# Performance work log

Measured on AMD Instinct MI355X. Metric: run time of the kernel, lower is better.

Reference implementation:

```python
import jax, jax.numpy as jnp
import numpy as np

B, T, D, H, V, L = 2, 1024, 512, 8, 50257, 4
HD = D // H  # head size
FF = 4 * D


def _ln(x, w, b):
    mu = jnp.mean(x, axis=-1, keepdims=True)
    var = jnp.mean((x - mu) ** 2, axis=-1, keepdims=True)
    return (x - mu) * jax.lax.rsqrt(var + 1e-5) * w + b


def setup_inputs() -> dict:
    key = jax.random.key(0)
    ks = jax.random.split(key, 12)
    s = 0.02
    return {
        "idx": jax.random.randint(ks[0], (B, T), 0, V),
        "tok_emb": jax.random.normal(ks[1], (V, D)) * s,
        "pos_emb": jax.random.normal(ks[2], (T, D)) * s,
        "Wq": jax.random.normal(ks[3], (L, H, D, HD)) * s,
        "Wk": jax.random.normal(ks[4], (L, H, D, HD)) * s,
        "Wv": jax.random.normal(ks[5], (L, H, D, HD)) * s,
        "Wo": jax.random.normal(ks[6], (L, D, D)) * s,
        "bo": jnp.zeros((L, D)),
        "W1": jax.random.normal(ks[7], (L, D, FF)) * s,
        "b1": jnp.zeros((L, FF)),
        "W2": jax.random.normal(ks[8], (L, FF, D)) * s,
        "b2": jnp.zeros((L, D)),
        "ln1_w": jnp.ones((L, D)), "ln1_b": jnp.zeros((L, D)),
        "ln2_w": jnp.ones((L, D)), "ln2_b": jnp.zeros((L, D)),
        "Wlm": jax.random.normal(ks[9], (D, V)) * s,
        "blm": jnp.zeros((V,)),
    }


def reference(idx, tok_emb, pos_emb, Wq, Wk, Wv, Wo, bo, W1, b1, W2, b2,
              ln1_w, ln1_b, ln2_w, ln2_b, Wlm, blm):
    b, t = idx.shape
    x = tok_emb[idx] + pos_emb[:t]  # [B,T,D]
    mask = jnp.tril(jnp.ones((t, t), dtype=bool))
    scale = D ** (-0.5)  # NOTE: original scales by full n_embd, not head_size
    for l in range(L):
        # pre-norm that also feeds the residual (x = ln1(x); x = x + sa(x))
        h = _ln(x, ln1_w[l], ln1_b[l])
        q = jnp.einsum('btd,hdk->bhtk', h, Wq[l])
        k = jnp.einsum('btd,hdk->bhtk', h, Wk[l])
        v = jnp.einsum('btd,hdk->bhtk', h, Wv[l])
        wei = jnp.einsum('bhtk,bhsk->bhts', q, k) * scale
        wei = jnp.where(mask, wei, -jnp.inf)
        wei = jax.nn.softmax(wei, axis=-1)  # dropout omitted (eval mode)
        att = jnp.einsum('bhts,bhsk->bhtk', wei, v)
        att = att.transpose(0, 2, 1, 3).reshape(b, t, D)  # concat heads
        x = h + att @ Wo[l] + bo[l]
        h2 = _ln(x, ln2_w[l], ln2_b[l])
        x = h2 + jax.nn.relu(h2 @ W1[l] + b1[l]) @ W2[l] + b2[l]
    logits = x @ Wlm + blm  # [B,T,V]
    return logits
```

## Files before the change

kernel.cpp:

```cpp
#include <hip/hip_runtime.h>
#include <hip/hip_bf16.h>

typedef __hip_bfloat16 bf16;
typedef __attribute__((ext_vector_type(8))) short s8v;
typedef __attribute__((ext_vector_type(4))) float f4v;

#define B_ 2
#define T_ 1024
#define D_ 512
#define H_ 8
#define HD_ 64
#define V_ 50257
#define VPAD_ 51200
#define L_ 4
#define FF_ 2048
#define BT_ (B_*T_)

__device__ __forceinline__ float ldw(const void* p, size_t i, int f32m) {
  return f32m ? ((const float*)p)[i] : __bfloat162float(((const bf16*)p)[i]);
}

__device__ __forceinline__ void gload_lds16(const void* g, void* l) {
  __builtin_amdgcn_global_load_lds((const __attribute__((address_space(1))) void*)g,
                                   (__attribute__((address_space(3))) void*)l, 16, 0, 0);
}

__global__ void detect_kernel(const void* __restrict__ ln1w, int* __restrict__ flag) {
  unsigned u = *(const unsigned*)ln1w;
  *flag = (u == 0x3F800000u) ? 1 : 0;
}

__global__ void embed_kernel(const int* __restrict__ idx, const void* __restrict__ tok,
                             const void* __restrict__ pos, float* __restrict__ x,
                             const int* __restrict__ flag) {
  int f32m = *flag;
  int i = blockIdx.x * 256 + threadIdx.x;
  int bt = i >> 9;
  int d  = i & (D_ - 1);
  int t  = bt & (T_ - 1);
  int tk = idx[bt];
  x[i] = ldw(tok, (size_t)tk * D_ + d, f32m) + ldw(pos, (size_t)t * D_ + d, f32m);
}

__global__ void ln_kernel(const float* __restrict__ x, const void* __restrict__ w,
                          const void* __restrict__ b, size_t eoff,
                          bf16* __restrict__ hb, float* __restrict__ hf,
                          const int* __restrict__ flag) {
  int f32m = *flag;
  int t = blockIdx.x;
  int tid = threadIdx.x;
  const float* row = x + (size_t)t * D_;
  float v0 = row[tid], v1 = row[tid + 256];
  __shared__ float red[256];
  red[tid] = v0 + v1;
  __syncthreads();
  for (int s = 128; s > 0; s >>= 1) { if (tid < s) red[tid] += red[tid + s]; __syncthreads(); }
  float mu = red[0] * (1.f / D_);
  __syncthreads();
  float d0 = v0 - mu, d1 = v1 - mu;
  red[tid] = d0 * d0 + d1 * d1;
  __syncthreads();
  for (int s = 128; s > 0; s >>= 1) { if (tid < s) red[tid] += red[tid + s]; __syncthreads(); }
  float rs = rsqrtf(red[0] * (1.f / D_) + 1e-5f);
  float o0 = d0 * rs * ldw(w, eoff + tid, f32m)       + ldw(b, eoff + tid, f32m);
  float o1 = d1 * rs * ldw(w, eoff + tid + 256, f32m) + ldw(b, eoff + tid + 256, f32m);
  size_t base = (size_t)t * D_;
  hf[base + tid] = o0;        hf[base + tid + 256] = o1;
  hb[base + tid] = __float2bfloat16(o0);
  hb[base + tid + 256] = __float2bfloat16(o1);
}

__global__ void repack_qkv_all_kernel(const void* __restrict__ Wq, const void* __restrict__ Wk,
                                      const void* __restrict__ Wv, bf16* __restrict__ out,
                                      const int* __restrict__ flag) {
  int f32m = *flag;
  int zz = blockIdx.z;
  size_t eoff = (size_t)zz * H_ * D_ * HD_;
  out += (size_t)zz * 1536 * 512;
  int i = blockIdx.x * 256 + threadIdx.x;
  int n = i >> 9, k = i & 511;
  int sel = n >> 9; int cc = n & 511; int hh = cc >> 6; int hd = cc & 63;
  const void* src = (sel == 0) ? Wq : (sel == 1) ? Wk : Wv;
  out[i] = __float2bfloat16(ldw(src, eoff + ((size_t)hh * D_ + k) * HD_ + hd, f32m));
}

__global__ void repack_qkv_kernel(const void* __restrict__ Wq, const void* __restrict__ Wk,
                                  const void* __restrict__ Wv, size_t eoff,
                                  bf16* __restrict__ out, const int* __restrict__ flag) {
  int f32m = *flag;
  int i = blockIdx.x * 256 + threadIdx.x;
  int n = i >> 9, k = i & 511;
  int sel = n >> 9; int cc = n & 511; int hh = cc >> 6; int hd = cc & 63;
  const void* src = (sel == 0) ? Wq : (sel == 1) ? Wk : Wv;
  out[i] = __float2bfloat16(ldw(src, eoff + ((size_t)hh * D_ + k) * HD_ + hd, f32m));
}

__global__ void transpose_kernel(const void* __restrict__ in, size_t eoff,
                                 bf16* __restrict__ out, int K, int Nin,
                                 const int* __restrict__ flag) {
  int f32m = *flag;
  __shared__ bf16 tl[32][33];
  int n0 = blockIdx.x * 32, k0 = blockIdx.y * 32;
  int tx = threadIdx.x & 31, ty = threadIdx.x >> 5;
#pragma unroll
  for (int i = 0; i < 4; ++i) {
    int k = k0 + ty + i * 8;
    int n = n0 + tx;
    float v = (n < Nin) ? ldw(in, eoff + (size_t)k * Nin + n, f32m) : 0.f;
    tl[ty + i * 8][tx] = __float2bfloat16(v);
  }
  __syncthreads();
#pragma unroll
  for (int i = 0; i < 4; ++i) {
    int n = n0 + ty + i * 8;
    out[(size_t)n * K + k0 + tx] = tl[tx][ty + i * 8];
  }
}

__global__ void transpose_all_kernel(const void* __restrict__ in,
                                     bf16* __restrict__ out,
                                     int K, int Nin, const int* __restrict__ flag) {
  int f32m = *flag;
  int zz = blockIdx.z;
  size_t eoff = (size_t)zz * K * Nin;
  out += (size_t)zz * Nin * K;
  __shared__ bf16 tl[32][33];
  int n0 = blockIdx.x * 32, k0 = blockIdx.y * 32;
  int tx = threadIdx.x & 31, ty = threadIdx.x >> 5;
#pragma unroll
  for (int i = 0; i < 4; ++i) {
    int k = k0 + ty + i * 8;
    int n = n0 + tx;
    tl[ty + i * 8][tx] = __float2bfloat16(ldw(in, eoff + (size_t)k * Nin + n, f32m));
  }
  __syncthreads();
#pragma unroll
  for (int i = 0; i < 4; ++i) {
    int n = n0 + ty + i * 8;
    out[(size_t)n * K + k0 + tx] = tl[tx][ty + i * 8];
  }
}

template<int OUTM, int BIAS, int RES, int RELU, int XB>
__global__ __launch_bounds__(256)
void mfma_gemm64(const bf16* __restrict__ A, const bf16* __restrict__ Bt,
                 void* __restrict__ Cout, const void* __restrict__ bias, size_t bieoff,
                 const float* __restrict__ res, bf16* __restrict__ xb2,
                 const int* __restrict__ flag, int M, int Nc, int K) {
  __shared__ __align__(16) short As[2][2048];
  __shared__ __align__(16) short Bs[2][2048];
  const int tid = threadIdx.x;
  const int brow = blockIdx.x * 64;
  const int bcol = blockIdx.y * 64;
  const int w = tid >> 6, lane = tid & 63;
  const int wr = w >> 1, wc = w & 1;
  const int lr = lane & 15, lk = lane >> 4;

  const int e0 = tid * 8;
  const int r0 = e0 >> 5;
  const int c0 = (e0 & 31) ^ ((r0 & 3) << 3);
  const bf16* ag0 = A + (size_t)(brow + r0) * K + c0;
  const bf16* bg0 = Bt + (size_t)(bcol + r0) * K + c0;

  int aoff[2], boff[2];
#pragma unroll
  for (int i = 0; i < 2; ++i) {
    int ra = wr * 32 + i * 16 + lr;
    aoff[i] = ra * 32 + ((lk * 8) ^ ((lr & 3) << 3));
    int rb = wc * 32 + i * 16 + lr;
    boff[i] = rb * 32 + ((lk * 8) ^ ((lr & 3) << 3));
  }

  f4v acc[2][2];
  const f4v z = {0.f, 0.f, 0.f, 0.f};
#pragma unroll
  for (int i = 0; i < 2; ++i)
#pragma unroll
    for (int j = 0; j < 2; ++j) acc[i][j] = z;

  const int nt = K >> 5;
  gload_lds16(ag0, &As[0][e0]);
  gload_lds16(bg0, &Bs[0][e0]);

  for (int kt = 0; kt < nt; ++kt) {
    __syncthreads();
    const int cur = kt & 1;
    if (kt + 1 < nt) {
      const size_t ko = (size_t)(kt + 1) * 32;
      gload_lds16(ag0 + ko, &As[cur ^ 1][e0]);
      gload_lds16(bg0 + ko, &Bs[cur ^ 1][e0]);
    }
    s8v a[2], b[2];
#pragma unroll
    for (int i = 0; i < 2; ++i) a[i] = *(const s8v*)&As[cur][aoff[i]];
#pragma unroll
    for (int i = 0; i < 2; ++i) b[i] = *(const s8v*)&Bs[cur][boff[i]];
#pragma unroll
    for (int mi = 0; mi < 2; ++mi)
#pragma unroll
      for (int ni = 0; ni < 2; ++ni)
        acc[mi][ni] = __builtin_amdgcn_mfma_f32_16x16x32_bf16(a[mi], b[ni], acc[mi][ni], 0, 0, 0);
  }

  const int f32m = *flag;
#pragma unroll
  for (int mi = 0; mi < 2; ++mi) {
    const int row = brow + wr * 32 + mi * 16 + lk * 4;
#pragma unroll
    for (int ni = 0; ni < 2; ++ni) {
      const int col = bcol + wc * 32 + ni * 16 + lr;
      if (col < Nc) {
        float bv = BIAS ? ldw(bias, bieoff + col, f32m) : 0.f;
#pragma unroll
        for (int rr = 0; rr < 4; ++rr) {
          float v = acc[mi][ni][rr] + bv;
          size_t ci = (size_t)(row + rr) * Nc + col;
          if (RES) v += res[ci];
          if (RELU) v = fmaxf(v, 0.f);
          if (OUTM == 0) ((float*)Cout)[ci] = v;
          else           ((bf16*)Cout)[ci] = __float2bfloat16(v);
          if (XB) xb2[ci] = __float2bfloat16(v);
        }
      }
    }
  }
}

__global__ __launch_bounds__(256)
void mfma_gemm_lm(const bf16* __restrict__ A, const bf16* __restrict__ Bt,
                  void* __restrict__ Cout, const void* __restrict__ bias,
                  const int* __restrict__ flag, int M, int Nc, int K) {
  __shared__ __align__(16) short As[2][4096];
  __shared__ __align__(16) short Bs[2][4096];
  const int bid = blockIdx.x;
  const int g = bid >> 3;
  const int brow = (g & 15) * 128;
  const int bcol = ((bid & 7) * 50 + (g >> 4)) * 128;
  const int tid = threadIdx.x;
  const int w = tid >> 6, lane = tid & 63;
  const int wr = w >> 1, wc = w & 1;
  const int lr = lane & 15, lk = lane >> 4;

  const int e0 = tid * 8, e1 = 2048 + tid * 8;
  const int r0 = e0 >> 5, r1 = e1 >> 5;
  const int c0 = (e0 & 31) ^ ((r0 & 3) << 3);
  const int c1 = (e1 & 31) ^ ((r1 & 3) << 3);
  const bf16* ag0 = A + (size_t)(brow + r0) * K + c0;
  const bf16* ag1 = A + (size_t)(brow + r1) * K + c1;
  const bf16* bg0 = Bt + (size_t)(bcol + r0) * K + c0;
  const bf16* bg1 = Bt + (size_t)(bcol + r1) * K + c1;

  int aoff[4], boff[4];
#pragma unroll
  for (int i = 0; i < 4; ++i) {
    int ra = wr * 64 + i * 16 + lr;
    aoff[i] = ra * 32 + ((lk * 8) ^ ((lr & 3) << 3));
    int rb = wc * 64 + i * 16 + lr;
    boff[i] = rb * 32 + ((lk * 8) ^ ((lr & 3) << 3));
  }

  f4v acc[4][4];
  const f4v z = {0.f, 0.f, 0.f, 0.f};
#pragma unroll
  for (int i = 0; i < 4; ++i)
#pragma unroll
    for (int j = 0; j < 4; ++j) acc[i][j] = z;

  const int nt = K >> 5;
  gload_lds16(ag0, &As[0][e0]); gload_lds16(ag1, &As[0][e1]);
  gload_lds16(bg0, &Bs[0][e0]); gload_lds16(bg1, &Bs[0][e1]);

  for (int kt = 0; kt < nt; ++kt) {
    __syncthreads();
    const int cur = kt & 1;
    if (kt + 1 < nt) {
      const size_t ko = (size_t)(kt + 1) * 32;
      gload_lds16(ag0 + ko, &As[cur ^ 1][e0]);
      gload_lds16(ag1 + ko, &As[cur ^ 1][e1]);
      gload_lds16(bg0 + ko, &Bs[cur ^ 1][e0]);
      gload_lds16(bg1 + ko, &Bs[cur ^ 1][e1]);
    }
    s8v a[4], b[4];
#pragma unroll
    for (int i = 0; i < 4; ++i) a[i] = *(const s8v*)&As[cur][aoff[i]];
#pragma unroll
    for (int i = 0; i < 4; ++i) b[i] = *(const s8v*)&Bs[cur][boff[i]];
#pragma unroll
    for (int mi = 0; mi < 4; ++mi)
#pragma unroll
      for (int ni = 0; ni < 4; ++ni)
        acc[mi][ni] = __builtin_amdgcn_mfma_f32_16x16x32_bf16(a[mi], b[ni], acc[mi][ni], 0, 0, 0);
  }

  const int f32m = *flag;
#pragma unroll
  for (int mi = 0; mi < 4; ++mi) {
    const int row = brow + wr * 64 + mi * 16 + lk * 4;
#pragma unroll
    for (int ni = 0; ni < 4; ++ni) {
      const int col = bcol + wc * 64 + ni * 16 + lr;
      if (col < Nc) {
        float bv = ldw(bias, col, f32m);
#pragma unroll
        for (int rr = 0; rr < 4; ++rr) {
          float v = acc[mi][ni][rr] + bv;
          size_t ci = (size_t)(row + rr) * Nc + col;
          if (f32m) ((float*)Cout)[ci] = v;
          else      ((bf16*)Cout)[ci] = __float2bfloat16(v);
        }
      }
    }
  }
}

#define ATT_SCALE 0.044194173824159216f
__global__ __launch_bounds__(128) void fattn_kernel(const bf16* __restrict__ qkv,
                                                    bf16* __restrict__ att) {
  const int tid = threadIdx.x;
  const int w = tid >> 6, lane = tid & 63;
  const int lr = lane & 15, lk = lane >> 4;
  const int sx = blockIdx.x;
  const int strip = (sx & 1) ? (31 - (sx >> 1)) : (sx >> 1);
  const int s0 = strip * 32;
  const int hh = blockIdx.y, b = blockIdx.z;
  const int q0w = s0 + w * 16;

  __shared__ __align__(16) short Klds[64 * 64];
  __shared__ __align__(16) short Vt[64 * 72];
  __shared__ __align__(16) short Pl[2][16 * 72];
  unsigned* vt32 = (unsigned*)Vt;

  const bf16* qbase = qkv + (size_t)(b * T_ + q0w + lr) * 1536 + hh * 64;
  s8v qf[2];
#pragma unroll
  for (int kk = 0; kk < 2; ++kk)
    qf[kk] = *(const s8v*)(qbase + kk * 32 + lk * 8);

  const bf16* kg = qkv + (size_t)b * T_ * 1536 + 512 + hh * 64;
  const bf16* vg = kg + 512;

  f4v acc_o[4];
  const f4v z4 = {0.f, 0.f, 0.f, 0.f};
#pragma unroll
  for (int dt = 0; dt < 4; ++dt) acc_o[dt] = z4;
  float m[4], l[4];
#pragma unroll
  for (int r = 0; r < 4; ++r) { m[r] = -1e30f; l[r] = 0.f; }

  const int jmax = (s0 + 31) >> 6;
  for (int jt = 0; jt <= jmax; ++jt) {
    __syncthreads();
    const bf16* kt = kg + (size_t)jt * 64 * 1536;
#pragma unroll
    for (int c = 0; c < 4; ++c) {
      int e = tid * 8 + c * 1024;
      int row = e >> 6, col = e & 63;
      int colw = col ^ ((row & 7) << 3);
      gload_lds16(kt + (size_t)row * 1536 + colw, &Klds[e]);
    }
    const bf16* vgt = vg + (size_t)jt * 64 * 1536;
#pragma unroll
    for (int u = 0; u < 2; ++u) {
      int unit = tid * 2 + u;
      int kp = unit >> 3, cc = (unit & 7) * 8;
      s8v v0 = *(const s8v*)(vgt + (size_t)(2 * kp) * 1536 + cc);
      s8v v1 = *(const s8v*)(vgt + (size_t)(2 * kp + 1) * 1536 + cc);
#pragma unroll
      for (int j = 0; j < 8; ++j) {
        unsigned pk = (unsigned)(unsigned short)v0[j] |
                      ((unsigned)(unsigned short)v1[j] << 16);
        vt32[(cc + j) * 36 + kp] = pk;
      }
    }
    __syncthreads();

    if (jt * 64 <= q0w + 15) {
      const bool diag = (jt == jmax);
      f4v s[4];
#pragma unroll
      for (int nt = 0; nt < 4; ++nt) s[nt] = z4;
#pragma unroll
      for (int kk = 0; kk < 2; ++kk)
#pragma unroll
        for (int nt = 0; nt < 4; ++nt) {
          int row = nt * 16 + lr;
          const s8v kf = *(const s8v*)&Klds[row * 64 +
                           ((kk * 32 + lk * 8) ^ ((lr & 7) << 3))];
          s[nt] = __builtin_amdgcn_mfma_f32_16x16x32_bf16(qf[kk], kf, s[nt], 0, 0, 0);
        }
      float pv[4][4];
#pragma unroll
      for (int nt = 0; nt < 4; ++nt)
#pragma unroll
        for (int r = 0; r < 4; ++r) {
          float v = s[nt][r] * ATT_SCALE;
          if (diag && (jt * 64 + nt * 16 + lr > q0w + lk * 4 + r)) v = -1e30f;
          pv[nt][r] = v;
        }
#pragma unroll
      for (int r = 0; r < 4; ++r) {
        float mm = fmaxf(fmaxf(pv[0][r], pv[1][r]), fmaxf(pv[2][r], pv[3][r]));
        mm = fmaxf(mm, __shfl_xor(mm, 1));
        mm = fmaxf(mm, __shfl_xor(mm, 2));
        mm = fmaxf(mm, __shfl_xor(mm, 4));
        mm = fmaxf(mm, __shfl_xor(mm, 8));
        float nm = fmaxf(m[r], mm);
        float cf = __expf(m[r] - nm);
        m[r] = nm;
        float ls = 0.f;
#pragma unroll
        for (int nt = 0; nt < 4; ++nt) {
          float p = __expf(pv[nt][r] - nm);
          pv[nt][r] = p;
          ls += p;
        }
        ls += __shfl_xor(ls, 1); ls += __shfl_xor(ls, 2);
        ls += __shfl_xor(ls, 4); ls += __shfl_xor(ls, 8);
        l[r] = l[r] * cf + ls;
#pragma unroll
        for (int dt = 0; dt < 4; ++dt) acc_o[dt][r] *= cf;
      }
      bf16* pw = (bf16*)&Pl[w][0];
#pragma unroll
      for (int nt = 0; nt < 4; ++nt)
#pragma unroll
        for (int r = 0; r < 4; ++r)
          pw[(lk * 4 + r) * 72 + nt * 16 + lr] = __float2bfloat16(pv[nt][r]);
#pragma unroll
      for (int kk = 0; kk < 2; ++kk) {
        const s8v pa = *(const s8v*)&Pl[w][lr * 72 + kk * 32 + lk * 8];
#pragma unroll
        for (int dt = 0; dt < 4; ++dt) {
          const s8v vf = *(const s8v*)&Vt[(dt * 16 + lr) * 72 + kk * 32 + lk * 8];
          acc_o[dt] = __builtin_amdgcn_mfma_f32_16x16x32_bf16(pa, vf, acc_o[dt], 0, 0, 0);
        }
      }
    }
  }

#pragma unroll
  for (int dt = 0; dt < 4; ++dt)
#pragma unroll
    for (int r = 0; r < 4; ++r) {
      int q = q0w + lk * 4 + r;
      float v = acc_o[dt][r] / l[r];
      att[(size_t)(b * T_ + q) * D_ + hh * 64 + dt * 16 + lr] = __float2bfloat16(v);
    }
}

__global__ void cast_kernel(const float* __restrict__ x, bf16* __restrict__ xb) {
  int i = blockIdx.x * 256 + threadIdx.x;
  xb[i] = __float2bfloat16(x[i]);
}

__global__ void lm_fallback_kernel(const float* __restrict__ A, const void* __restrict__ Bw,
                                   void* __restrict__ Cout, const void* __restrict__ bias,
                                   const int* __restrict__ flag, int M, int N, int K) {
  const int f32m = *flag;
  __shared__ __align__(16) float As[16][72];
  __shared__ __align__(16) float Bs[16][72];
  const int tid = threadIdx.x;
  const int brow = blockIdx.y * 64;
  const int bcol = blockIdx.x * 64;
  const int tr = tid >> 4, tc = tid & 15;
  float acc[4][4] = {};
  for (int k0 = 0; k0 < K; k0 += 16) {
#pragma unroll
    for (int i = 0; i < 4; ++i) {
      int e = tid + i * 256;
      int r = e >> 4, c = e & 15;
      As[c][r] = A[(size_t)(brow + r) * K + k0 + c];
    }
#pragma unroll
    for (int i = 0; i < 4; ++i) {
      int e = tid + i * 256;
      int r = e >> 6, c = e & 63;
      int col = bcol + c;
      Bs[r][c] = (col < N) ? ldw(Bw, (size_t)(k0 + r) * N + col, f32m) : 0.f;
    }
    __syncthreads();
#pragma unroll
    for (int kk = 0; kk < 16; ++kk) {
      const float4 av = *reinterpret_cast<const float4*>(&As[kk][tr * 4]);
      const float4 bv = *reinterpret_cast<const float4*>(&Bs[kk][tc * 4]);
      float a_[4] = {av.x, av.y, av.z, av.w};
      float b_[4] = {bv.x, bv.y, bv.z, bv.w};
#pragma unroll
      for (int i = 0; i < 4; ++i)
#pragma unroll
        for (int j = 0; j < 4; ++j) acc[i][j] += a_[i] * b_[j];
    }
    __syncthreads();
  }
#pragma unroll
  for (int i = 0; i < 4; ++i) {
    int row = brow + tr * 4 + i;
#pragma unroll
    for (int j = 0; j < 4; ++j) {
      int col = bcol + tc * 4 + j;
      if (col < N) {
        float v = acc[i][j] + ldw(bias, col, f32m);
        if (f32m) ((float*)Cout)[(size_t)row * N + col] = v;
        else      ((bf16*) Cout)[(size_t)row * N + col] = __float2bfloat16(v);
      }
    }
  }
}

template<int OUTM, int BI, int RE, int RL, int XB>
static void launch_g64(const bf16* A, const bf16* Bt, void* C, const void* bias,
                       size_t bieoff, const float* res, bf16* xb2, const int* flag,
                       int M, int Nc, int Npad, int K, hipStream_t s) {
  dim3 grid(M / 64, Npad / 64);
  mfma_gemm64<OUTM, BI, RE, RL, XB><<<grid, 256, 0, s>>>(A, Bt, C, bias, bieoff, res,
                                                         xb2, flag, M, Nc, K);
}

extern "C" void kernel_launch(void* const* d_in, const int* in_sizes, int n_in,
                              void* d_out, int out_size, void* d_ws, size_t ws_size,
                              hipStream_t stream) {
  const int*  idx  = (const int*) d_in[0];
  const void* tok  = d_in[1];
  const void* pos  = d_in[2];
  const void* Wq   = d_in[3];
  const void* Wk   = d_in[4];
  const void* Wv   = d_in[5];
  const void* Wo   = d_in[6];
  const void* bo   = d_in[7];
  const void* W1   = d_in[8];
  const void* b1   = d_in[9];
  const void* W2   = d_in[10];
  const void* b2   = d_in[11];
  const void* ln1w = d_in[12];
  const void* ln1b = d_in[13];
  const void* ln2w = d_in[14];
  const void* ln2b = d_in[15];
  const void* Wlm  = d_in[16];
  const void* blm  = d_in[17];

  char* p = (char*)d_ws;
  int*   flag = (int*)p;            p += 256;
  float* x    = (float*)p;          p += (size_t)BT_ * D_ * 4;
  float* hf   = (float*)p;          p += (size_t)BT_ * D_ * 4;
  bf16*  h    = (bf16*)p;           p += (size_t)BT_ * D_ * 2;
  bf16*  R    = (bf16*)p;           p += (size_t)BT_ * FF_ * 2;
  bf16*  qkvP = (bf16*)p;           p += (size_t)L_ * 1536 * 512 * 2;
  bf16*  woP  = (bf16*)p;           p += (size_t)L_ * 512 * 512 * 2;
  bf16*  w1P  = (bf16*)p;           p += (size_t)L_ * 2048 * 512 * 2;
  bf16*  w2P  = (bf16*)p;           p += (size_t)L_ * 512 * 2048 * 2;
  bf16*  wlmP = (bf16*)p;
  size_t need_all = (size_t)(p - (char*)d_ws) + (size_t)VPAD_ * D_ * 2;
  bf16*  wrep = qkvP;
  bf16*  wlmF = (bf16*)((char*)qkvP + (size_t)FF_ * D_ * 2);
  size_t need_old = ((char*)wlmF - (char*)d_ws) + (size_t)VPAD_ * D_ * 2;

  bf16* qkv = R;
  bf16* att = R + (size_t)BT_ * 1536;
  bf16* ff  = R;
  bf16* xb  = h;

  detect_kernel<<<1, 1, 0, stream>>>(ln1w, flag);
  embed_kernel<<<BT_ * D_ / 256, 256, 0, stream>>>(idx, tok, pos, x, flag);

  if (ws_size >= need_all) {
    repack_qkv_all_kernel<<<dim3(1536 * 512 / 256, 1, L_), 256, 0, stream>>>(
        Wq, Wk, Wv, qkvP, flag);
    transpose_all_kernel<<<dim3(16, 16, L_), 256, 0, stream>>>(Wo, woP, 512, 512, flag);
    transpose_all_kernel<<<dim3(64, 16, L_), 256, 0, stream>>>(W1, w1P, 512, 2048, flag);
    transpose_all_kernel<<<dim3(16, 64, L_), 256, 0, stream>>>(W2, w2P, 2048, 512, flag);
    transpose_kernel<<<dim3(VPAD_ / 32, 16), 256, 0, stream>>>(Wlm, 0, wlmP, 512, V_, flag);

    for (int l = 0; l < L_; ++l) {
      ln_kernel<<<BT_, 256, 0, stream>>>(x, ln1w, ln1b, (size_t)l * D_, h, hf, flag);
      launch_g64<1,0,0,0,0>(h, qkvP + (size_t)l * 1536 * 512, qkv, nullptr, 0, nullptr,
                            nullptr, flag, BT_, 1536, 1536, 512, stream);
      fattn_kernel<<<dim3(32, H_, B_), 128, 0, stream>>>(qkv, att);
      launch_g64<0,1,1,0,0>(att, woP + (size_t)l * 512 * 512, x, bo, (size_t)l * D_, hf,
                            nullptr, flag, BT_, 512, 512, 512, stream);
      ln_kernel<<<BT_, 256, 0, stream>>>(x, ln2w, ln2b, (size_t)l * D_, h, hf, flag);
      launch_g64<1,1,0,1,0>(h, w1P + (size_t)l * 2048 * 512, ff, b1, (size_t)l * FF_,
                            nullptr, nullptr, flag, BT_, 2048, 2048, 512, stream);
      if (l < L_ - 1)
        launch_g64<0,1,1,0,0>(ff, w2P + (size_t)l * 512 * 2048, x, b2, (size_t)l * D_, hf,
                              nullptr, flag, BT_, 512, 512, 2048, stream);
      else
        launch_g64<0,1,1,0,1>(ff, w2P + (size_t)l * 512 * 2048, x, b2, (size_t)l * D_, hf,
                              xb, flag, BT_, 512, 512, 2048, stream);
    }
    mfma_gemm_lm<<<(BT_ / 128) * (VPAD_ / 128), 256, 0, stream>>>(
        xb, wlmP, d_out, blm, flag, BT_, V_, 512);
  } else {
    const bool big = ws_size >= need_old;
    for (int l = 0; l < L_; ++l) {
      ln_kernel<<<BT_, 256, 0, stream>>>(x, ln1w, ln1b, (size_t)l * D_, h, hf, flag);
      repack_qkv_kernel<<<1536 * 512 / 256, 256, 0, stream>>>(
          Wq, Wk, Wv, (size_t)l * H_ * D_ * HD_, wrep, flag);
      launch_g64<1,0,0,0,0>(h, wrep, qkv, nullptr, 0, nullptr, nullptr, flag,
                            BT_, 1536, 1536, 512, stream);
      fattn_kernel<<<dim3(32, H_, B_), 128, 0, stream>>>(qkv, att);
      transpose_kernel<<<dim3(16, 16), 256, 0, stream>>>(Wo, (size_t)l * D_ * D_, wrep, 512, 512, flag);
      launch_g64<0,1,1,0,0>(att, wrep, x, bo, (size_t)l * D_, hf, nullptr, flag,
                            BT_, 512, 512, 512, stream);
      ln_kernel<<<BT_, 256, 0, stream>>>(x, ln2w, ln2b, (size_t)l * D_, h, hf, flag);
      transpose_kernel<<<dim3(64, 16), 256, 0, stream>>>(W1, (size_t)l * D_ * FF_, wrep, 512, 2048, flag);
      launch_g64<1,1,0,1,0>(h, wrep, ff, b1, (size_t)l * FF_, nullptr, nullptr, flag,
                            BT_, 2048, 2048, 512, stream);
      transpose_kernel<<<dim3(16, 64), 256, 0, stream>>>(W2, (size_t)l * FF_ * D_, wrep, 2048, 512, flag);
      launch_g64<0,1,1,0,0>(ff, wrep, x, b2, (size_t)l * D_, hf, nullptr, flag,
                            BT_, 512, 512, 2048, stream);
    }
    if (big) {
      cast_kernel<<<BT_ * D_ / 256, 256, 0, stream>>>(x, xb);
      transpose_kernel<<<dim3(VPAD_ / 32, 16), 256, 0, stream>>>(Wlm, 0, wlmF, 512, V_, flag);
      mfma_gemm_lm<<<(BT_ / 128) * (VPAD_ / 128), 256, 0, stream>>>(
          xb, wlmF, d_out, blm, flag, BT_, V_, 512);
    } else {
      lm_fallback_kernel<<<dim3((V_ + 63) / 64, BT_ / 64), 256, 0, stream>>>(
          x, Wlm, d_out, blm, flag, BT_, V_, 512);
    }
  }
}
```

Measured before the change: 774.4 us.

## Use 256x256 tiles with 4-stage LDS pipeline for LM-head GEMM

Replaces the 128x128, 256-thread LM-head GEMM with a 256x256 tile kernel using 512 threads, a 4-deep LDS buffer ring with explicit vmcnt waits, and raised wave priority around the MFMA block. Larger tiles raise arithmetic intensity per loaded byte, and the deeper prefetch is meant to hide global-load latency. The XCD-aware block mapping and LDS swizzle are adjusted to match. It uses 128KB of LDS and many accumulator registers, so occupancy is limited to one block per CU, and K is now hardcoded to 512.

```diff
diff --git a/kernel.cpp b/kernel.cpp
--- a/kernel.cpp
+++ b/kernel.cpp
@@ -226,76 +226,89 @@
   }
 }
 
-__global__ __launch_bounds__(256)
-void mfma_gemm_lm(const bf16* __restrict__ A, const bf16* __restrict__ Bt,
-                  void* __restrict__ Cout, const void* __restrict__ bias,
-                  const int* __restrict__ flag, int M, int Nc, int K) {
-  __shared__ __align__(16) short As[2][4096];
-  __shared__ __align__(16) short Bs[2][4096];
+__global__ __launch_bounds__(512, 1)
+void mfma_gemm_lm256(const bf16* __restrict__ A, const bf16* __restrict__ Bt,
+                     void* __restrict__ Cout, const void* __restrict__ bias,
+                     const int* __restrict__ flag, int M, int Nc) {
+  const int K = 512;
+  __shared__ __align__(16) short As[4][8192];
+  __shared__ __align__(16) short Bs[4][8192];
   const int bid = blockIdx.x;
-  const int g = bid >> 3;
-  const int brow = (g & 15) * 128;
-  const int bcol = ((bid & 7) * 50 + (g >> 4)) * 128;
+  const int xcd = bid & 7;
+  const int chunk = bid >> 3;
+  const int brow = (chunk & 7) * 256;
+  const int bcol = (xcd * 25 + (chunk >> 3)) * 256;
   const int tid = threadIdx.x;
   const int w = tid >> 6, lane = tid & 63;
-  const int wr = w >> 1, wc = w & 1;
+  const int wr = w >> 2, wc = w & 3;
   const int lr = lane & 15, lk = lane >> 4;
 
-  const int e0 = tid * 8, e1 = 2048 + tid * 8;
+  const int e0 = tid * 8, e1 = 4096 + tid * 8;
   const int r0 = e0 >> 5, r1 = e1 >> 5;
-  const int c0 = (e0 & 31) ^ ((r0 & 3) << 3);
-  const int c1 = (e1 & 31) ^ ((r1 & 3) << 3);
+  const int c0 = (e0 & 31) ^ (((r0 >> 1) & 3) << 3);
+  const int c1 = (e1 & 31) ^ (((r1 >> 1) & 3) << 3);
   const bf16* ag0 = A + (size_t)(brow + r0) * K + c0;
   const bf16* ag1 = A + (size_t)(brow + r1) * K + c1;
   const bf16* bg0 = Bt + (size_t)(bcol + r0) * K + c0;
   const bf16* bg1 = Bt + (size_t)(bcol + r1) * K + c1;
 
-  int aoff[4], boff[4];
-#pragma unroll
-  for (int i = 0; i < 4; ++i) {
-    int ra = wr * 64 + i * 16 + lr;
-    aoff[i] = ra * 32 + ((lk * 8) ^ ((lr & 3) << 3));
-    int rb = wc * 64 + i * 16 + lr;
-    boff[i] = rb * 32 + ((lk * 8) ^ ((lr & 3) << 3));
-  }
-
-  f4v acc[4][4];
+  int aoff[8], boff[4];
+#pragma unroll
+  for (int mi = 0; mi < 8; ++mi) {
+    int ra = wr * 128 + mi * 16 + lr;
+    aoff[mi] = ra * 32 + ((lk * 8) ^ (((ra >> 1) & 3) << 3));
+  }
+#pragma unroll
+  for (int ni = 0; ni < 4; ++ni) {
+    int rb = wc * 64 + ni * 16 + lr;
+    boff[ni] = rb * 32 + ((lk * 8) ^ (((rb >> 1) & 3) << 3));
+  }
+
+  f4v acc[8][4];
   const f4v z = {0.f, 0.f, 0.f, 0.f};
 #pragma unroll
-  for (int i = 0; i < 4; ++i)
+  for (int i = 0; i < 8; ++i)
 #pragma unroll
     for (int j = 0; j < 4; ++j) acc[i][j] = z;
 
-  const int nt = K >> 5;
-  gload_lds16(ag0, &As[0][e0]); gload_lds16(ag1, &As[0][e1]);
-  gload_lds16(bg0, &Bs[0][e0]); gload_lds16(bg1, &Bs[0][e1]);
-
-  for (int kt = 0; kt < nt; ++kt) {
-    __syncthreads();
-    const int cur = kt & 1;
-    if (kt + 1 < nt) {
-      const size_t ko = (size_t)(kt + 1) * 32;
-      gload_lds16(ag0 + ko, &As[cur ^ 1][e0]);
-      gload_lds16(ag1 + ko, &As[cur ^ 1][e1]);
-      gload_lds16(bg0 + ko, &Bs[cur ^ 1][e0]);
-      gload_lds16(bg1 + ko, &Bs[cur ^ 1][e1]);
-    }
-    s8v a[4], b[4];
-#pragma unroll
-    for (int i = 0; i < 4; ++i) a[i] = *(const s8v*)&As[cur][aoff[i]];
+#pragma unroll
+  for (int t = 0; t < 3; ++t) {
+    const size_t ko = (size_t)t * 32;
+    gload_lds16(ag0 + ko, &As[t][e0]); gload_lds16(ag1 + ko, &As[t][e1]);
+    gload_lds16(bg0 + ko, &Bs[t][e0]); gload_lds16(bg1 + ko, &Bs[t][e1]);
+  }
+
+  for (int kt = 0; kt < 16; ++kt) {
+    if (kt < 14)       asm volatile("s_waitcnt vmcnt(8)" ::: "memory");
+    else if (kt == 14) asm volatile("s_waitcnt vmcnt(4)" ::: "memory");
+    else               asm volatile("s_waitcnt vmcnt(0)" ::: "memory");
+    __builtin_amdgcn_s_barrier();
+    __builtin_amdgcn_sched_barrier(0);
+    const int cur = kt & 3;
+    if (kt + 3 < 16) {
+      const int nb = (kt + 3) & 3;
+      const size_t ko = (size_t)(kt + 3) * 32;
+      gload_lds16(ag0 + ko, &As[nb][e0]); gload_lds16(ag1 + ko, &As[nb][e1]);
+      gload_lds16(bg0 + ko, &Bs[nb][e0]); gload_lds16(bg1 + ko, &Bs[nb][e1]);
+    }
+    s8v a[8], b[4];
+#pragma unroll
+    for (int i = 0; i < 8; ++i) a[i] = *(const s8v*)&As[cur][aoff[i]];
 #pragma unroll
     for (int i = 0; i < 4; ++i) b[i] = *(const s8v*)&Bs[cur][boff[i]];
-#pragma unroll
-    for (int mi = 0; mi < 4; ++mi)
+    __builtin_amdgcn_s_setprio(1);
+#pragma unroll
+    for (int mi = 0; mi < 8; ++mi)
 #pragma unroll
       for (int ni = 0; ni < 4; ++ni)
         acc[mi][ni] = __builtin_amdgcn_mfma_f32_16x16x32_bf16(a[mi], b[ni], acc[mi][ni], 0, 0, 0);
+    __builtin_amdgcn_s_setprio(0);
   }
 
   const int f32m = *flag;
 #pragma unroll
-  for (int mi = 0; mi < 4; ++mi) {
-    const int row = brow + wr * 64 + mi * 16 + lk * 4;
+  for (int mi = 0; mi < 8; ++mi) {
+    const int row = brow + wr * 128 + mi * 16 + lk * 4;
 #pragma unroll
     for (int ni = 0; ni < 4; ++ni) {
       const int col = bcol + wc * 64 + ni * 16 + lr;
@@ -587,8 +600,8 @@
         launch_g64<0,1,1,0,1>(ff, w2P + (size_t)l * 512 * 2048, x, b2, (size_t)l * D_, hf,
                               xb, flag, BT_, 512, 512, 2048, stream);
     }
-    mfma_gemm_lm<<<(BT_ / 128) * (VPAD_ / 128), 256, 0, stream>>>(
-        xb, wlmP, d_out, blm, flag, BT_, V_, 512);
+    mfma_gemm_lm256<<<(BT_ / 256) * (VPAD_ / 256), 512, 0, stream>>>(
+        xb, wlmP, d_out, blm, flag, BT_, V_);
   } else {
     const bool big = ws_size >= need_old;
     for (int l = 0; l < L_; ++l) {
@@ -612,8 +625,8 @@
     if (big) {
       cast_kernel<<<BT_ * D_ / 256, 256, 0, stream>>>(x, xb);
       transpose_kernel<<<dim3(VPAD_ / 32, 16), 256, 0, stream>>>(Wlm, 0, wlmF, 512, V_, flag);
-      mfma_gemm_lm<<<(BT_ / 128) * (VPAD_ / 128), 256, 0, stream>>>(
-          xb, wlmF, d_out, blm, flag, BT_, V_, 512);
+      mfma_gemm_lm256<<<(BT_ / 256) * (VPAD_ / 256), 512, 0, stream>>>(
+          xb, wlmF, d_out, blm, flag, BT_, V_);
     } else {
       lm_fallback_kernel<<<dim3((V_ + 63) / 64, BT_ / 64), 256, 0, stream>>>(
           x, Wlm, d_out, blm, flag, BT_, V_, 512);
```

Result: no change. 776.1 us (+0.2%).
